# Kernel optimization log

Measured on AMD Instinct MI355X. Metric: run time of the kernel, lower is better.

The kernel has to match this reference:

```python
import jax, jax.numpy as jnp
import numpy as np

B, T, D, H = 4, 2048, 1024, 16
DK = DV = 64
R = 64
KS = 4
EPS = 1e-6


def setup_inputs() -> dict:
    key = jax.random.key(0)
    ks = jax.random.split(key, 16)
    def w(k, shape, s=0.02):
        return jax.random.normal(k, shape, jnp.float32) * s
    return {
        "x": jax.random.normal(ks[0], (B, T, D), jnp.float32),
        "conv_q_w": w(ks[1], (D, 1, KS), 0.3), "conv_q_b": jnp.zeros((D,), jnp.float32),
        "conv_k_w": w(ks[2], (D, 1, KS), 0.3), "conv_k_b": jnp.zeros((D,), jnp.float32),
        "conv_v_w": w(ks[3], (D, 1, KS), 0.3), "conv_v_b": jnp.zeros((D,), jnp.float32),
        "Wq": w(ks[4], (D, H * DK)), "bq": jnp.zeros((H * DK,), jnp.float32),
        "Wk": w(ks[5], (D, H * DK)), "bk": jnp.zeros((H * DK,), jnp.float32),
        "Wv": w(ks[6], (D, H * DV)), "bv": jnp.zeros((H * DV,), jnp.float32),
        "W_ad": w(ks[7], (D, R)), "b_ad": jnp.zeros((R,), jnp.float32),
        "W_au": w(ks[8], (R, H * DK)), "b_au": jnp.zeros((H * DK,), jnp.float32),
        "W_beta": w(ks[9], (D, H)), "b_beta": jnp.zeros((H,), jnp.float32),
        "rms_w": jnp.ones((H, DV), jnp.float32),
        "W_gd": w(ks[10], (D, R)), "b_gd": jnp.zeros((R,), jnp.float32),
        "W_gu": w(ks[11], (R, H)), "b_gu": jnp.zeros((H,), jnp.float32),
        "Wo": w(ks[12], (H * DV, D)), "bo": jnp.zeros((D,), jnp.float32),
    }


def _shortconv(x, w, b):
    # causal depthwise conv1d: torch pads (KS-1) both sides then slices [:T] == left-pad KS-1
    xc = jnp.transpose(x, (0, 2, 1))  # [B, D, T]
    y = jax.lax.conv_general_dilated(
        xc, w, (1,), [(KS - 1, 0)],
        dimension_numbers=("NCH", "OIH", "NCH"), feature_group_count=D)
    y = y + b[None, :, None]
    return jax.nn.silu(jnp.transpose(y, (0, 2, 1)))  # [B, T, D]


def _l2(x):
    # x / sqrt(clamp(sum(x^2), eps))  (matches torch clamp_min then sqrt)
    return x / jnp.sqrt(jnp.maximum(jnp.sum(x * x, -1, keepdims=True), EPS))


def _heads(z, dh):
    # [B,T,H*dh] -> [B*H,T,dh]
    return jnp.transpose(z.reshape(B, T, H, dh), (0, 2, 1, 3)).reshape(B * H, T, dh)


def reference(x, conv_q_w, conv_q_b, conv_k_w, conv_k_b, conv_v_w, conv_v_b,
              Wq, bq, Wk, bk, Wv, bv, W_ad, b_ad, W_au, b_au, W_beta, b_beta,
              rms_w, W_gd, b_gd, W_gu, b_gu, Wo, bo):
    qx = _shortconv(x, conv_q_w, conv_q_b)
    kx = _shortconv(x, conv_k_w, conv_k_b)
    vx = _shortconv(x, conv_v_w, conv_v_b)
    Q = _l2(_heads(qx @ Wq + bq, DK))            # [BH,T,DK]
    K = _l2(_heads(kx @ Wk + bk, DK))            # [BH,T,DK]
    V = _heads(vx @ Wv + bv, DV)                 # [BH,T,DV]
    alpha = jax.nn.sigmoid(jax.nn.silu(x @ W_ad + b_ad) @ W_au + b_au)  # [B,T,H*DK]
    A = _heads(alpha, DK)                        # [BH,T,DK]
    beta = jax.nn.sigmoid(x @ W_beta + b_beta)   # [B,T,H]
    Bta = jnp.transpose(beta, (0, 2, 1)).reshape(B * H, T, 1)

    S0 = jnp.zeros((B * H, DK, DV), jnp.float32)

    def step(S, inp):
        q, k, v, a, b = inp                      # [BH,DK],[BH,DK],[BH,DV],[BH,DK],[BH,1]
        S = S * a[:, :, None]                    # gated decay (row scale)
        kTS = jnp.einsum("bi,bij->bj", k, S)    # k^T S : [BH,DV]
        S = S + (b * k)[:, :, None] * (v - kTS)[:, None, :]  # rank-1 delta update
        o = jnp.einsum("bij,bi->bj", S, q)      # S^T q : [BH,DV]
        return S, o

    tm = lambda z: jnp.transpose(z, (1, 0, 2))   # time-major for scan
    S_final, out_t = jax.lax.scan(step, S0, (tm(Q), tm(K), tm(V), tm(A), tm(Bta)))
    O = jnp.transpose(out_t, (1, 0, 2)).reshape(B, H, T, DV)

    # headwise RMSNorm then sigmoid output gate
    var = jnp.mean(O * O, -1, keepdims=True)
    O = O * jax.lax.rsqrt(var + EPS) * rms_w[None, :, None, :]
    gate = jax.nn.sigmoid(jax.nn.silu(x @ W_gd + b_gd) @ W_gu + b_gu)  # [B,T,H]
    O = O * jnp.transpose(gate, (0, 2, 1))[:, :, :, None]

    y = jnp.transpose(O, (0, 2, 1, 3)).reshape(B, T, H * DV) @ Wo + bo
    return y, S_final.reshape(B, H, DK, DV)
```

## Files before the change

kernel.cpp:

```cpp
#include <hip/hip_runtime.h>
#include <hip/hip_bf16.h>
#include <cstdint>

#define BB 4
#define TT 2048
#define DD 1024
#define HH 16
#define NR (BB*TT)
#define CC 16
#define NCH (TT/CC)

typedef __attribute__((ext_vector_type(8))) short bf16x8;
typedef __attribute__((ext_vector_type(4))) float f32x4;
typedef __attribute__((ext_vector_type(2))) float f32x2;
typedef __attribute__((ext_vector_type(4))) unsigned int u32x4;
typedef __attribute__((ext_vector_type(2))) unsigned int u32x2;

#define GLL(g, l, SZ) __builtin_amdgcn_global_load_lds( \
    (const __attribute__((address_space(1))) void*)(uintptr_t)(const void*)(g), \
    (__attribute__((address_space(3))) void*)(uintptr_t)(void*)(l), SZ, 0, 0)

__device__ __forceinline__ unsigned short f2bf(float f) {
  unsigned u = __builtin_bit_cast(unsigned, f);
  unsigned r = 0x7FFFu + ((u >> 16) & 1u);
  return (unsigned short)((u + r) >> 16);
}
__device__ __forceinline__ unsigned pk2(float a, float b) {
  return (unsigned)f2bf(a) | ((unsigned)f2bf(b) << 16);
}
__device__ __forceinline__ float siluf(float v) { return v / (1.f + __expf(-v)); }
__device__ __forceinline__ float sigmf(float v) { return 1.f / (1.f + __expf(-v)); }

__global__ __launch_bounds__(256) void prep_weights(
    const float* __restrict__ Wq, const float* __restrict__ Wk,
    const float* __restrict__ Wv, const float* __restrict__ Wo,
    unsigned short* __restrict__ WqT, unsigned short* __restrict__ WkT,
    unsigned short* __restrict__ WvT, unsigned short* __restrict__ WoT,
    const float* __restrict__ Wau, unsigned short* __restrict__ WauT,
    const float* __restrict__ Wad, const float* __restrict__ Wgd,
    const float* __restrict__ Wbeta, unsigned short* __restrict__ Wst1T,
    const float* __restrict__ Wgu, unsigned short* __restrict__ WguT,
    const float* __restrict__ bad, const float* __restrict__ bgd,
    const float* __restrict__ bbeta, const float* __restrict__ bgu,
    float* __restrict__ bst1, float* __restrict__ bgup) {
  const int blk = (int)blockIdx.x;
  const int tid = threadIdx.x;
  if (blk < 1024) {
    __shared__ float tile[64][65];
    const int which = blk >> 8, sub = blk & 255;
    const float* W = (which == 0) ? Wq : (which == 1) ? Wk : (which == 2) ? Wv : Wo;
    unsigned short* Wt = (which == 0) ? WqT : (which == 1) ? WkT : (which == 2) ? WvT : WoT;
    const int bk = (sub & 15) * 64, bn = (sub >> 4) * 64;
    const int r = tid >> 2, c4 = (tid & 3) * 16;
#pragma unroll 4
    for (int e = 0; e < 16; ++e)
      tile[r][c4 + e] = W[(size_t)(bk + r) * 1024 + bn + c4 + e];
    __syncthreads();
#pragma unroll 4
    for (int e = 0; e < 16; ++e)
      Wt[(size_t)(bn + r) * 1024 + bk + c4 + e] = f2bf(tile[c4 + e][r]);
  } else if (blk < 1280) {
    int idx = (blk - 1024) * 256 + tid;
    int n = idx >> 6, k = idx & 63;
    WauT[idx] = f2bf(Wau[(size_t)k * 1024 + n]);
  } else if (blk < 2304) {
    int idx = (blk - 1280) * 256 + tid;
    int n = idx >> 10, k = idx & 1023;
    float v = 0.f;
    if (n < 64) v = Wad[(size_t)k * 64 + n];
    else if (n < 128) v = Wgd[(size_t)k * 64 + (n - 64)];
    else if (n < 144) v = Wbeta[(size_t)k * 16 + (n - 128)];
    Wst1T[idx] = f2bf(v);
  } else if (blk < 2336) {
    int idx = (blk - 2304) * 256 + tid;
    int n = idx >> 6, k = idx & 63;
    float v = (n < 16) ? Wgu[(size_t)k * 16 + n] : 0.f;
    WguT[idx] = f2bf(v);
  } else {
    float v = 0.f;
    if (tid < 64) v = bad[tid];
    else if (tid < 128) v = bgd[tid - 64];
    else if (tid < 144) v = bbeta[tid - 128];
    bst1[tid] = v;
    if (tid < 128) bgup[tid] = (tid < 16) ? bgu[tid] : 0.f;
  }
}

__global__ __launch_bounds__(256) void conv_silu(
    const float* __restrict__ x,
    const float* __restrict__ qw, const float* __restrict__ qb,
    const float* __restrict__ kw, const float* __restrict__ kb,
    const float* __restrict__ vw, const float* __restrict__ vb,
    unsigned short* __restrict__ qx, unsigned short* __restrict__ kx,
    unsigned short* __restrict__ vx, unsigned short* __restrict__ xb) {
  const int n = blockIdx.x;
  const int t = n & (TT - 1);
  const int d0 = threadIdx.x * 4;
  const size_t base = (size_t)n * DD + d0;
  f32x4 zero = {0.f, 0.f, 0.f, 0.f};
  f32x4 x0 = *(const f32x4*)(x + base);
  f32x4 xm1 = (t >= 1) ? *(const f32x4*)(x + base - DD) : zero;
  f32x4 xm2 = (t >= 2) ? *(const f32x4*)(x + base - 2 * DD) : zero;
  f32x4 xm3 = (t >= 3) ? *(const f32x4*)(x + base - 3 * DD) : zero;
  float sq[4], sk[4], sv[4];
#pragma unroll
  for (int e = 0; e < 4; ++e) {
    const int d = d0 + e;
    const f32x4 wq = *(const f32x4*)(qw + (size_t)d * 4);
    const f32x4 wk = *(const f32x4*)(kw + (size_t)d * 4);
    const f32x4 wv = *(const f32x4*)(vw + (size_t)d * 4);
    float aq = wq[0] * xm3[e] + wq[1] * xm2[e] + wq[2] * xm1[e] + wq[3] * x0[e] + qb[d];
    float ak = wk[0] * xm3[e] + wk[1] * xm2[e] + wk[2] * xm1[e] + wk[3] * x0[e] + kb[d];
    float av = wv[0] * xm3[e] + wv[1] * xm2[e] + wv[2] * xm1[e] + wv[3] * x0[e] + vb[d];
    sq[e] = siluf(aq); sk[e] = siluf(ak); sv[e] = siluf(av);
  }
  u32x2 o;
  o[0] = pk2(sq[0], sq[1]); o[1] = pk2(sq[2], sq[3]); *(u32x2*)(qx + base) = o;
  o[0] = pk2(sk[0], sk[1]); o[1] = pk2(sk[2], sk[3]); *(u32x2*)(kx + base) = o;
  o[0] = pk2(sv[0], sv[1]); o[1] = pk2(sv[2], sv[3]); *(u32x2*)(vx + base) = o;
  o[0] = pk2(x0[0], x0[1]); o[1] = pk2(x0[2], x0[3]); *(u32x2*)(xb + base) = o;
}

template <int ACT>
__global__ __launch_bounds__(256) void gemm_bt(
    const unsigned short* __restrict__ A, const unsigned short* __restrict__ Bt,
    const float* __restrict__ bias, float* __restrict__ C,
    int M, int N, int K, int ldc, int nstore) {
  __shared__ unsigned short lsA[128 * 32];
  __shared__ unsigned short lsB[128 * 32];
  const int tid = threadIdx.x;
  const int wid = tid >> 6, lane = tid & 63;
  const int wr = wid >> 1, wc = wid & 1;
  int bx = blockIdx.x, by = blockIdx.y;
  {
    const int nwg = gridDim.x * gridDim.y;
    if ((nwg & 7) == 0) {
      const int flat = by * gridDim.x + bx;
      const int cpx = nwg >> 3;
      const int nf = (flat & 7) * cpx + (flat >> 3);
      bx = nf % gridDim.x;
      by = nf / gridDim.x;
    }
  }
  const int m0 = bx * 128, n0 = by * 128;
  f32x4 acc[4][4] = {};
  const int nk = K >> 5;
  const int r0 = wid * 32 + (lane >> 2);
  const int cb = (lane & 3) * 16;
  char* lA = (char*)lsA;
  char* lB = (char*)lsB;
  const size_t rowb = (size_t)K * 2;

  for (int kt = 0; kt < nk; ++kt) {
    const char* gA = (const char*)(A + (size_t)(m0 + r0) * K) + kt * 64 + cb;
    const char* gB = (const char*)(Bt + (size_t)(n0 + r0) * K) + kt * 64 + cb;
    GLL(gA, lA + (wid * 32) * 64, 16);
    GLL(gA + 16 * rowb, lA + (wid * 32 + 16) * 64, 16);
    GLL(gB, lB + (wid * 32) * 64, 16);
    GLL(gB + 16 * rowb, lB + (wid * 32 + 16) * 64, 16);
    __syncthreads();
    bf16x8 af[4], bfr[4];
#pragma unroll
    for (int f = 0; f < 4; ++f)
      af[f] = *(const bf16x8*)(lA + (wr * 64 + f * 16 + (lane & 15)) * 64 + (lane >> 4) * 16);
#pragma unroll
    for (int f = 0; f < 4; ++f)
      bfr[f] = *(const bf16x8*)(lB + (wc * 64 + f * 16 + (lane & 15)) * 64 + (lane >> 4) * 16);
#pragma unroll
    for (int i = 0; i < 4; ++i)
#pragma unroll
      for (int j = 0; j < 4; ++j)
        acc[i][j] = __builtin_amdgcn_mfma_f32_16x16x32_bf16(af[i], bfr[j], acc[i][j], 0, 0, 0);
    __syncthreads();
  }

  if (ACT == 2) {
#pragma unroll
    for (int i = 0; i < 4; ++i) {
      float ss[4] = {0.f, 0.f, 0.f, 0.f};
#pragma unroll
      for (int j = 0; j < 4; ++j) {
        const int gc = n0 + wc * 64 + j * 16 + (lane & 15);
        const float bv = bias[gc];
#pragma unroll
        for (int r = 0; r < 4; ++r) {
          float v = acc[i][j][r] + bv;
          acc[i][j][r] = v;
          ss[r] = fmaf(v, v, ss[r]);
        }
      }
#pragma unroll
      for (int r = 0; r < 4; ++r) {
        float s = ss[r];
        s += __shfl_xor(s, 1);
        s += __shfl_xor(s, 2);
        s += __shfl_xor(s, 4);
        s += __shfl_xor(s, 8);
        ss[r] = 1.f / sqrtf(fmaxf(s, 1e-6f));
      }
      const int gr0 = m0 + wr * 64 + i * 16 + (lane >> 4) * 4;
#pragma unroll
      for (int j = 0; j < 4; ++j) {
        const int gc = n0 + wc * 64 + j * 16 + (lane & 15);
#pragma unroll
        for (int r = 0; r < 4; ++r)
          C[(size_t)(gr0 + r) * ldc + gc] = acc[i][j][r] * ss[r];
      }
    }
    return;
  }

#pragma unroll
  for (int i = 0; i < 4; ++i) {
    const int gr0 = m0 + wr * 64 + i * 16 + (lane >> 4) * 4;
#pragma unroll
    for (int j = 0; j < 4; ++j) {
      const int gc = n0 + wc * 64 + j * 16 + (lane & 15);
      if (gc < nstore) {
        const float bv = bias[gc];
#pragma unroll
        for (int r = 0; r < 4; ++r) {
          float v = acc[i][j][r] + bv;
          if (ACT == 1) v = sigmf(v);
          C[(size_t)(gr0 + r) * ldc + gc] = v;
        }
      }
    }
  }
}

__global__ __launch_bounds__(256) void gemm_stage1(
    const unsigned short* __restrict__ A, const unsigned short* __restrict__ Bt,
    const float* __restrict__ bias,
    unsigned short* __restrict__ adb, unsigned short* __restrict__ gdb,
    float* __restrict__ betaT) {
  __shared__ unsigned short lsA[128 * 32];
  __shared__ unsigned short lsB[128 * 32];
  const int tid = threadIdx.x;
  const int wid = tid >> 6, lane = tid & 63;
  const int wr = wid >> 1, wc = wid & 1;
  int bx = blockIdx.x, by = blockIdx.y;
  {
    const int nwg = gridDim.x * gridDim.y;
    const int flat = by * gridDim.x + bx;
    const int cpx = nwg >> 3;
    const int nf = (flat & 7) * cpx + (flat >> 3);
    bx = nf % gridDim.x;
    by = nf / gridDim.x;
  }
  const int m0 = bx * 128, n0 = by * 128;
  const int K = 1024;
  f32x4 acc[4][4] = {};
  const int r0 = wid * 32 + (lane >> 2);
  const int cb = (lane & 3) * 16;
  char* lA = (char*)lsA;
  char* lB = (char*)lsB;
  const size_t rowb = (size_t)K * 2;

  for (int kt = 0; kt < 32; ++kt) {
    const char* gA = (const char*)(A + (size_t)(m0 + r0) * K) + kt * 64 + cb;
    const char* gB = (const char*)(Bt + (size_t)(n0 + r0) * K) + kt * 64 + cb;
    GLL(gA, lA + (wid * 32) * 64, 16);
    GLL(gA + 16 * rowb, lA + (wid * 32 + 16) * 64, 16);
    GLL(gB, lB + (wid * 32) * 64, 16);
    GLL(gB + 16 * rowb, lB + (wid * 32 + 16) * 64, 16);
    __syncthreads();
    bf16x8 af[4], bfr[4];
#pragma unroll
    for (int f = 0; f < 4; ++f)
      af[f] = *(const bf16x8*)(lA + (wr * 64 + f * 16 + (lane & 15)) * 64 + (lane >> 4) * 16);
#pragma unroll
    for (int f = 0; f < 4; ++f)
      bfr[f] = *(const bf16x8*)(lB + (wc * 64 + f * 16 + (lane & 15)) * 64 + (lane >> 4) * 16);
#pragma unroll
    for (int i = 0; i < 4; ++i)
#pragma unroll
      for (int j = 0; j < 4; ++j)
        acc[i][j] = __builtin_amdgcn_mfma_f32_16x16x32_bf16(af[i], bfr[j], acc[i][j], 0, 0, 0);
    __syncthreads();
  }

#pragma unroll
  for (int i = 0; i < 4; ++i) {
    const int gr0 = m0 + wr * 64 + i * 16 + (lane >> 4) * 4;
#pragma unroll
    for (int j = 0; j < 4; ++j) {
      const int gc = n0 + wc * 64 + j * 16 + (lane & 15);
      if (gc >= 144) continue;
      const float bv = bias[gc];
#pragma unroll
      for (int r = 0; r < 4; ++r) {
        const int row = gr0 + r;
        float v = acc[i][j][r] + bv;
        if (gc < 64) {
          adb[(size_t)row * 64 + gc] = f2bf(siluf(v));
        } else if (gc < 128) {
          gdb[(size_t)row * 64 + (gc - 64)] = f2bf(siluf(v));
        } else {
          int bb = row >> 11, tt = row & (TT - 1);
          betaT[((size_t)(bb * HH + (gc - 128))) * TT + tt] = sigmf(v);
        }
      }
    }
  }
}

__global__ __launch_bounds__(256) void scan_phaseA(
    float* __restrict__ Qn, float* __restrict__ Kn, float* __restrict__ Vv,
    float* __restrict__ Alp, const float* __restrict__ betaT,
    float* __restrict__ Pbuf, float* __restrict__ bCbuf) {
  __shared__ float bA[CC][68], bKt[CC][68], bKp[CC][68], bQ[CC][68];
  __shared__ float bW1[CC][68], bW2[CC][68], bU1[CC][68], bU2[CC][68];
  __shared__ float Nm[CC][20], Nt[CC][20];
  __shared__ float bet[CC];
  const int bid = (int)blockIdx.x;
  const int bh = bid >> 7, c = bid & 127;
  const int b = bh >> 4, h = bh & 15;
  const int tid = threadIdx.x;
  const int tG = tid >> 4, sA = tid & 15, dG = sA * 4;
  const size_t seg = ((size_t)b * TT) * DD + h * 64;
  const size_t off = seg + (size_t)(c * CC + tG) * DD + dG;

  *(f32x4*)&bA [tG][dG] = *(const f32x4*)(Alp + off);
  *(f32x4*)&bKt[tG][dG] = *(const f32x4*)(Kn  + off);
  *(f32x4*)&bW1[tG][dG] = *(const f32x4*)(Vv  + off);
  *(f32x4*)&bQ [tG][dG] = *(const f32x4*)(Qn  + off);
  if (tid < CC) bet[tid] = betaT[(size_t)bh * TT + c * CC + tid];
  __syncthreads();

  if (tid < 64) {
    float p = bA[0][tid];
#pragma unroll
    for (int t = 1; t < CC; ++t) { p *= bA[t][tid]; bA[t][tid] = p; }
  }
  __syncthreads();

  {
    f32x4 bb = *(f32x4*)&bA[tG][dG];
    f32x4 kk = *(f32x4*)&bKt[tG][dG];
    f32x4 qq = *(f32x4*)&bQ[tG][dG];
    f32x4 vv = *(f32x4*)&bW1[tG][dG];
    f32x4 bC = *(f32x4*)&bA[CC - 1][dG];
    const float bt = bet[tG];
    f32x4 kt, kp, qt, w1, w2, kb;
#pragma unroll
    for (int e = 0; e < 4; ++e) {
      float inv = 1.0f / bb[e];
      kt[e] = kk[e] * bb[e];
      kp[e] = kk[e] * inv;
      qt[e] = qq[e] * bb[e];
      w1[e] = bt * vv[e];
      w2[e] = bt * kt[e];
      kb[e] = kp[e] * bC[e];
    }
    *(f32x4*)&bKt[tG][dG] = kt;
    *(f32x4*)&bKp[tG][dG] = kp;
    *(f32x4*)&bQ [tG][dG] = qt;
    *(f32x4*)&bW1[tG][dG] = w1;
    *(f32x4*)&bW2[tG][dG] = w2;
    *(f32x4*)(Qn + off) = qt;
    *(f32x4*)(Alp + off) = kb;
    if (tid < 64) bCbuf[((size_t)bh * 128 + c) * 64 + tid] = bA[CC - 1][tid];
  }
  __syncthreads();

  {
    f32x4 da = {0.f, 0.f, 0.f, 0.f}, dp = {0.f, 0.f, 0.f, 0.f};
#pragma unroll
    for (int ii = 0; ii < 16; ++ii) {
      f32x4 y = *(f32x4*)&bKp[sA][ii * 4];
      da += (*(f32x4*)&bKt[tG][ii * 4]) * y;
      dp += (*(f32x4*)&bQ [tG][ii * 4]) * y;
    }
    float dotA = (da[0] + da[1]) + (da[2] + da[3]);
    float dotP = (dp[0] + dp[1]) + (dp[2] + dp[3]);
    Nm[tG][sA] = (sA < tG) ? (-bet[tG] * dotA) : 0.f;
    Pbuf[((size_t)bh * 128 + c) * 256 + tG * 16 + sA] = (sA <= tG) ? dotP : 0.f;
  }
  __syncthreads();

#define NEUM2(Pw, I1, I2, O1, O2)                                        \
    {                                                                    \
      f32x4 a1 = *(f32x4*)&I1[tG][dG];                                   \
      f32x4 a2 = *(f32x4*)&I2[tG][dG];                                   \
      for (int s4 = 0; s4 < 4; ++s4) {                                   \
        f32x4 pv = *(f32x4*)&Pw[tG][s4 * 4];                             \
        _Pragma("unroll")                                                \
        for (int e = 0; e < 4; ++e) {                                    \
          a1 += pv[e] * (*(f32x4*)&I1[s4 * 4 + e][dG]);                  \
          a2 += pv[e] * (*(f32x4*)&I2[s4 * 4 + e][dG]);                  \
        }                                                                \
      }                                                                  \
      *(f32x4*)&O1[tG][dG] = a1;                                         \
      *(f32x4*)&O2[tG][dG] = a2;                                         \
    }
#define SQMAT(Pw, Pout)                                                  \
    {                                                                    \
      float acc = 0.f;                                                   \
      _Pragma("unroll")                                                  \
      for (int s = 0; s < 16; ++s) acc = fmaf(Pw[tG][s], Pw[s][sA], acc);\
      Pout[tG][sA] = acc;                                                \
    }

  NEUM2(Nm, bW1, bW2, bU1, bU2)
  SQMAT(Nm, Nt)
  __syncthreads();
  NEUM2(Nt, bU1, bU2, bW1, bW2)
  SQMAT(Nt, Nm)
  __syncthreads();
  NEUM2(Nm, bW1, bW2, bU1, bU2)
  SQMAT(Nm, Nt)
  __syncthreads();
  {
    f32x4 a1 = *(f32x4*)&bU1[tG][dG];
    f32x4 a2 = *(f32x4*)&bU2[tG][dG];
    for (int s4 = 0; s4 < 4; ++s4) {
      f32x4 pv = *(f32x4*)&Nt[tG][s4 * 4];
#pragma unroll
      for (int e = 0; e < 4; ++e) {
        a1 += pv[e] * (*(f32x4*)&bU1[s4 * 4 + e][dG]);
        a2 += pv[e] * (*(f32x4*)&bU2[s4 * 4 + e][dG]);
      }
    }
    *(f32x4*)(Vv + off) = a1;
    *(f32x4*)(Kn + off) = a2;
  }
#undef NEUM2
#undef SQMAT
}

__global__ __launch_bounds__(512, 2) void scan_phaseB(
    const float* __restrict__ W1g, const float* __restrict__ W2g,
    const float* __restrict__ Qt, const float* __restrict__ Kb,
    const float* __restrict__ Pbuf, const float* __restrict__ bCbuf,
    float* __restrict__ O, float* __restrict__ Sout) {
  __shared__ float S0T[16][68];
  __shared__ float pU [16][17][2];
  __shared__ float pOq[16][17][2];
  __shared__ float pw2[2][16][68];
  __shared__ float pqt[2][16][68];
  __shared__ float pkb[2][16][68];
  __shared__ float pP [2][16][20];
  __shared__ float pbC[2][64];
  const int blk = (int)blockIdx.x;
  const int bh = blk & 63, cg = blk >> 6;
  const int b = bh >> 4, hh = bh & 15;
  const int tid = threadIdx.x;
  const int h = tid >> 8;
  const int t8 = tid & 255;
  const int T = t8 >> 4, j = t8 & 15;
  const int jg = cg * 16 + j;
  const size_t seg = ((size_t)b * TT) * DD + hh * 64;

  const int qr = t8 >> 4, qc = t8 & 15;

#define PLOAD(c, W2R, QTR, KBR, PR, BCR, W1R)                               \
  {                                                                         \
    const size_t rb = seg + (size_t)((c) * CC + qr) * DD + qc * 4;          \
    if (h == 0) {                                                           \
      W2R = *(const f32x4*)(W2g + rb);                                      \
      QTR = *(const f32x4*)(Qt + rb);                                       \
      W1R = W1g[seg + (size_t)((c) * CC + T) * DD + jg];                    \
    } else {                                                                \
      KBR = *(const f32x4*)(Kb + rb);                                       \
      PR  = Pbuf[((size_t)bh * 128 + (c)) * 256 + t8];                      \
      BCR = (t8 < 64) ? bCbuf[((size_t)bh * 128 + (c)) * 64 + t8] : 0.f;    \
    }                                                                       \
  }
#define PSTORE(bufI, W2R, QTR, KBR, PR, BCR)                                \
  {                                                                         \
    if (h == 0) {                                                           \
      *(f32x4*)&pw2[bufI][qr][qc * 4] = W2R;                                \
      *(f32x4*)&pqt[bufI][qr][qc * 4] = QTR;                                \
    } else {                                                                \
      *(f32x4*)&pkb[bufI][qr][qc * 4] = KBR;                                \
      pP[bufI][qr][qc] = PR;                                                \
      if (t8 < 64) pbC[bufI][t8] = BCR;                                     \
    }                                                                       \
  }

  f32x4 w2r = {}, qtr = {}, kbr = {};
  float pr = 0.f, bcr = 0.f, w1l = 0.f;
  PLOAD(0, w2r, qtr, kbr, pr, bcr, w1l)
  PSTORE(0, w2r, qtr, kbr, pr, bcr)
  {
    int e0 = tid, e1 = tid + 512;
    S0T[e0 >> 6][e0 & 63] = 0.f;
    S0T[e1 >> 6][e1 & 63] = 0.f;
  }
  __syncthreads();

  for (int c = 0; c < NCH; ++c) {
    const int buf = c & 1;
    f32x4 w2n = {}, qtn = {}, kbn = {};
    float pn = 0.f, bcn = 0.f, w1n = 0.f;
    const bool more = (c + 1 < NCH);
    if (more) PLOAD(c + 1, w2n, qtn, kbn, pn, bcn, w1n)

    float u0 = (h == 0) ? w1l : 0.f, u1 = 0.f, q0 = 0.f, q1 = 0.f;
#pragma unroll
    for (int k4 = 0; k4 < 8; ++k4) {
      const int kk = h * 32 + k4 * 4;
      f32x4 wv = *(const f32x4*)&pw2[buf][T][kk];
      f32x4 qv = *(const f32x4*)&pqt[buf][T][kk];
      f32x4 sv = *(const f32x4*)&S0T[j][kk];
      u0 = fmaf(-wv[0], sv[0], u0); q0 = fmaf(qv[0], sv[0], q0);
      u1 = fmaf(-wv[1], sv[1], u1); q1 = fmaf(qv[1], sv[1], q1);
      u0 = fmaf(-wv[2], sv[2], u0); q0 = fmaf(qv[2], sv[2], q0);
      u1 = fmaf(-wv[3], sv[3], u1); q1 = fmaf(qv[3], sv[3], q1);
    }
    pU[T][j][h] = u0 + u1;
    pOq[T][j][h] = q0 + q1;
    __syncthreads();

    float um[CC];
#pragma unroll
    for (int s = 0; s < CC; ++s) {
      f32x2 t2 = *(const f32x2*)&pU[s][j][0];
      um[s] = t2[0] + t2[1];
    }

    if (h == 0) {
      f32x2 oq2 = *(const f32x2*)&pOq[T][j][0];
      float o = oq2[0] + oq2[1];
#pragma unroll
      for (int s4 = 0; s4 < 4; ++s4) {
        f32x4 pv = *(const f32x4*)&pP[buf][T][s4 * 4];
        o = fmaf(pv[0], um[s4 * 4 + 0], o);
        o = fmaf(pv[1], um[s4 * 4 + 1], o);
        o = fmaf(pv[2], um[s4 * 4 + 2], o);
        o = fmaf(pv[3], um[s4 * 4 + 3], o);
      }
      O[seg + (size_t)(c * CC + T) * DD + jg] = o;
    }

    {
      const int r0 = 4 * T + 2 * h;
      f32x2 bcv = *(const f32x2*)&pbC[buf][r0];
      f32x2 s2 = *(const f32x2*)&S0T[j][r0];
      float sp0 = bcv[0] * s2[0];
      float sp1 = bcv[1] * s2[1];
#pragma unroll
      for (int s = 0; s < CC; ++s) {
        f32x2 kv = *(const f32x2*)&pkb[buf][s][r0];
        sp0 = fmaf(kv[0], um[s], sp0);
        sp1 = fmaf(kv[1], um[s], sp1);
      }
      f32x2 so = {sp0, sp1};
      *(f32x2*)&S0T[j][r0] = so;
    }

    if (more) PSTORE(buf ^ 1, w2n, qtn, kbn, pn, bcn)
    __syncthreads();
    w1l = w1n;
  }
#undef PLOAD
#undef PSTORE

  {
    const int r0 = 4 * T + 2 * h;
    f32x2 s2 = *(const f32x2*)&S0T[j][r0];
    Sout[(size_t)bh * 4096 + (size_t)(r0 + 0) * 64 + jg] = s2[0];
    Sout[(size_t)bh * 4096 + (size_t)(r0 + 1) * 64 + jg] = s2[1];
  }
}

__global__ __launch_bounds__(256) void rms_gate(
    const float* __restrict__ O, const float* __restrict__ rmsw,
    const float* __restrict__ gate, unsigned short* __restrict__ Og) {
  const int tid = threadIdx.x;
  const int row = blockIdx.x * 4 + (tid >> 6);
  const int lane = tid & 63;
  const int h = lane >> 2;
  const float* p = O + (size_t)row * DD + lane * 16;
  f32x4 v[4];
  float ss = 0.f;
#pragma unroll
  for (int u = 0; u < 4; ++u) {
    v[u] = *(const f32x4*)(p + u * 4);
#pragma unroll
    for (int e = 0; e < 4; ++e) ss = fmaf(v[u][e], v[u][e], ss);
  }
  ss += __shfl_xor(ss, 1);
  ss += __shfl_xor(ss, 2);
  const float rs = rsqrtf(ss * (1.f / 64.f) + 1e-6f);
  const float g = gate[row * 16 + h];
  const float* wp = rmsw + h * 64 + (lane & 3) * 16;
  unsigned ow[8];
#pragma unroll
  for (int u = 0; u < 4; ++u) {
    f32x4 wv = *(const f32x4*)(wp + u * 4);
    float a0 = v[u][0] * rs * wv[0] * g, a1 = v[u][1] * rs * wv[1] * g;
    float a2 = v[u][2] * rs * wv[2] * g, a3 = v[u][3] * rs * wv[3] * g;
    ow[u * 2] = pk2(a0, a1);
    ow[u * 2 + 1] = pk2(a2, a3);
  }
  u32x4* dst = (u32x4*)(Og + (size_t)row * DD + lane * 16);
  u32x4 o1, o2;
  o1[0] = ow[0]; o1[1] = ow[1]; o1[2] = ow[2]; o1[3] = ow[3];
  o2[0] = ow[4]; o2[1] = ow[5]; o2[2] = ow[6]; o2[3] = ow[7];
  dst[0] = o1; dst[1] = o2;
}

extern "C" void kernel_launch(void* const* d_in, const int* in_sizes, int n_in,
                              void* d_out, int out_size, void* d_ws, size_t ws_size,
                              hipStream_t stream) {
  const float* x    = (const float*)d_in[0];
  const float* qw   = (const float*)d_in[1];
  const float* qb   = (const float*)d_in[2];
  const float* kw   = (const float*)d_in[3];
  const float* kb   = (const float*)d_in[4];
  const float* vw   = (const float*)d_in[5];
  const float* vb   = (const float*)d_in[6];
  const float* Wq   = (const float*)d_in[7];
  const float* bq   = (const float*)d_in[8];
  const float* Wk   = (const float*)d_in[9];
  const float* bk   = (const float*)d_in[10];
  const float* Wv   = (const float*)d_in[11];
  const float* bv   = (const float*)d_in[12];
  const float* Wad  = (const float*)d_in[13];
  const float* bad  = (const float*)d_in[14];
  const float* Wau  = (const float*)d_in[15];
  const float* bau  = (const float*)d_in[16];
  const float* Wbeta= (const float*)d_in[17];
  const float* bbeta= (const float*)d_in[18];
  const float* rmsw = (const float*)d_in[19];
  const float* Wgd  = (const float*)d_in[20];
  const float* bgd  = (const float*)d_in[21];
  const float* Wgu  = (const float*)d_in[22];
  const float* bgu  = (const float*)d_in[23];
  const float* Wo   = (const float*)d_in[24];
  const float* bo   = (const float*)d_in[25];

  char* ws = (char*)d_ws;
  const size_t MB = 1ull << 20;
  unsigned short* WqT   = (unsigned short*)(ws + 0 * MB);
  unsigned short* WkT   = (unsigned short*)(ws + 2 * MB);
  unsigned short* WvT   = (unsigned short*)(ws + 4 * MB);
  unsigned short* WoT   = (unsigned short*)(ws + 6 * MB);
  unsigned short* WauT  = (unsigned short*)(ws + 8 * MB);
  unsigned short* Wst1T = (unsigned short*)(ws + 8 * MB + 256 * 1024);
  unsigned short* WguT  = (unsigned short*)(ws + 8 * MB + 768 * 1024);
  float* bst1 = (float*)(ws + 8 * MB + 800 * 1024);
  float* bgup = (float*)(ws + 8 * MB + 804 * 1024);
  unsigned short* x_bf = (unsigned short*)(ws + 9 * MB);
  unsigned short* qx   = (unsigned short*)(ws + 25 * MB);
  unsigned short* kx   = (unsigned short*)(ws + 41 * MB);
  unsigned short* vx   = (unsigned short*)(ws + 57 * MB);
  float* Qn    = (float*)(ws + 73 * MB);
  float* Kn    = (float*)(ws + 105 * MB);
  float* Vv    = (float*)(ws + 137 * MB);
  float* stage1= (float*)(ws + 169 * MB);
  unsigned short* adb = (unsigned short*)(ws + 177 * MB);
  unsigned short* gdb = (unsigned short*)(ws + 178 * MB);
  float* betaT = (float*)(ws + 179 * MB);
  float* gate  = (float*)(ws + 179 * MB + 512 * 1024);
  float* bCbuf = (float*)(ws + 180 * MB);
  float* alpha = (float*)(ws + 9 * MB);
  float* Obuf  = (float*)(ws + 41 * MB);
  unsigned short* Og = (unsigned short*)(ws + 137 * MB);
  float* Pbuf  = stage1;
  float* y = (float*)d_out;
  float* Sout = y + (size_t)NR * DD;

  dim3 blk(256);
  prep_weights<<<dim3(2337), blk, 0, stream>>>(
      Wq, Wk, Wv, Wo, WqT, WkT, WvT, WoT,
      Wau, WauT, Wad, Wgd, Wbeta, Wst1T, Wgu, WguT,
      bad, bgd, bbeta, bgu, bst1, bgup);

  conv_silu<<<dim3(NR), blk, 0, stream>>>(x, qw, qb, kw, kb, vw, vb, qx, kx, vx, x_bf);

  gemm_stage1<<<dim3(64, 2), blk, 0, stream>>>(x_bf, Wst1T, bst1, adb, gdb, betaT);
  gemm_bt<2><<<dim3(64, 8), blk, 0, stream>>>(qx, WqT, bq, Qn, NR, 1024, 1024, 1024, 1024);
  gemm_bt<2><<<dim3(64, 8), blk, 0, stream>>>(kx, WkT, bk, Kn, NR, 1024, 1024, 1024, 1024);
  gemm_bt<0><<<dim3(64, 8), blk, 0, stream>>>(vx, WvT, bv, Vv, NR, 1024, 1024, 1024, 1024);
  gemm_bt<1><<<dim3(64, 8), blk, 0, stream>>>(adb, WauT, bau, alpha, NR, 1024, 64, 1024, 1024);
  gemm_bt<1><<<dim3(64, 1), blk, 0, stream>>>(gdb, WguT, bgup, gate, NR, 128, 64, 16, 16);

  scan_phaseA<<<dim3(8192), blk, 0, stream>>>(Qn, Kn, Vv, alpha, betaT, Pbuf, bCbuf);
  scan_phaseB<<<dim3(256), dim3(512), 0, stream>>>(Vv, Kn, Qn, alpha, Pbuf, bCbuf, Obuf, Sout);

  rms_gate<<<dim3(2048), blk, 0, stream>>>(Obuf, rmsw, gate, Og);
  gemm_bt<0><<<dim3(64, 8), blk, 0, stream>>>(Og, WoT, bo, y, NR, 1024, 1024, 1024, 1024);
}
```

Before: 492.3 us.

## Fuse conv into weight prep kernel and form chunk inverse before applying

Merges the depthwise conv/SiLU kernel into the weight-prep kernel as one launch, which saves a kernel launch and its tail. In phase A, the Neumann-series inverse (I+N)^-1 is now built as a 16x16 matrix by repeated squaring. It is then applied once to W1/W2, instead of multiplying the 16x64 operands at every step. This cuts LDS traffic and FLOPs in the triangular solve and frees two shared buffers, with a small change in floating-point summation order.

```diff
diff --git a/kernel.cpp b/kernel.cpp
--- a/kernel.cpp
+++ b/kernel.cpp
@@ -31,7 +31,13 @@
 __device__ __forceinline__ float siluf(float v) { return v / (1.f + __expf(-v)); }
 __device__ __forceinline__ float sigmf(float v) { return 1.f / (1.f + __expf(-v)); }
 
-__global__ __launch_bounds__(256) void prep_weights(
+__global__ __launch_bounds__(256) void prologue(
+    const float* __restrict__ x,
+    const float* __restrict__ qw, const float* __restrict__ qb,
+    const float* __restrict__ kw, const float* __restrict__ kb,
+    const float* __restrict__ vw, const float* __restrict__ vb,
+    unsigned short* __restrict__ qx, unsigned short* __restrict__ kx,
+    unsigned short* __restrict__ vx, unsigned short* __restrict__ xb,
     const float* __restrict__ Wq, const float* __restrict__ Wk,
     const float* __restrict__ Wv, const float* __restrict__ Wo,
     unsigned short* __restrict__ WqT, unsigned short* __restrict__ WkT,
@@ -43,8 +49,38 @@
     const float* __restrict__ bad, const float* __restrict__ bgd,
     const float* __restrict__ bbeta, const float* __restrict__ bgu,
     float* __restrict__ bst1, float* __restrict__ bgup) {
-  const int blk = (int)blockIdx.x;
+  const int blk0 = (int)blockIdx.x;
   const int tid = threadIdx.x;
+  if (blk0 < NR) {
+    const int n = blk0;
+    const int t = n & (TT - 1);
+    const int d0 = tid * 4;
+    const size_t base = (size_t)n * DD + d0;
+    f32x4 zero = {0.f, 0.f, 0.f, 0.f};
+    f32x4 x0 = *(const f32x4*)(x + base);
+    f32x4 xm1 = (t >= 1) ? *(const f32x4*)(x + base - DD) : zero;
+    f32x4 xm2 = (t >= 2) ? *(const f32x4*)(x + base - 2 * DD) : zero;
+    f32x4 xm3 = (t >= 3) ? *(const f32x4*)(x + base - 3 * DD) : zero;
+    float sq[4], sk[4], sv[4];
+#pragma unroll
+    for (int e = 0; e < 4; ++e) {
+      const int d = d0 + e;
+      const f32x4 wq = *(const f32x4*)(qw + (size_t)d * 4);
+      const f32x4 wk = *(const f32x4*)(kw + (size_t)d * 4);
+      const f32x4 wv = *(const f32x4*)(vw + (size_t)d * 4);
+      float aq = wq[0] * xm3[e] + wq[1] * xm2[e] + wq[2] * xm1[e] + wq[3] * x0[e] + qb[d];
+      float ak = wk[0] * xm3[e] + wk[1] * xm2[e] + wk[2] * xm1[e] + wk[3] * x0[e] + kb[d];
+      float av = wv[0] * xm3[e] + wv[1] * xm2[e] + wv[2] * xm1[e] + wv[3] * x0[e] + vb[d];
+      sq[e] = siluf(aq); sk[e] = siluf(ak); sv[e] = siluf(av);
+    }
+    u32x2 o;
+    o[0] = pk2(sq[0], sq[1]); o[1] = pk2(sq[2], sq[3]); *(u32x2*)(qx + base) = o;
+    o[0] = pk2(sk[0], sk[1]); o[1] = pk2(sk[2], sk[3]); *(u32x2*)(kx + base) = o;
+    o[0] = pk2(sv[0], sv[1]); o[1] = pk2(sv[2], sv[3]); *(u32x2*)(vx + base) = o;
+    o[0] = pk2(x0[0], x0[1]); o[1] = pk2(x0[2], x0[3]); *(u32x2*)(xb + base) = o;
+    return;
+  }
+  const int blk = blk0 - NR;
   if (blk < 1024) {
     __shared__ float tile[64][65];
     const int which = blk >> 8, sub = blk & 255;
@@ -86,41 +122,6 @@
   }
 }
 
-__global__ __launch_bounds__(256) void conv_silu(
-    const float* __restrict__ x,
-    const float* __restrict__ qw, const float* __restrict__ qb,
-    const float* __restrict__ kw, const float* __restrict__ kb,
-    const float* __restrict__ vw, const float* __restrict__ vb,
-    unsigned short* __restrict__ qx, unsigned short* __restrict__ kx,
-    unsigned short* __restrict__ vx, unsigned short* __restrict__ xb) {
-  const int n = blockIdx.x;
-  const int t = n & (TT - 1);
-  const int d0 = threadIdx.x * 4;
-  const size_t base = (size_t)n * DD + d0;
-  f32x4 zero = {0.f, 0.f, 0.f, 0.f};
-  f32x4 x0 = *(const f32x4*)(x + base);
-  f32x4 xm1 = (t >= 1) ? *(const f32x4*)(x + base - DD) : zero;
-  f32x4 xm2 = (t >= 2) ? *(const f32x4*)(x + base - 2 * DD) : zero;
-  f32x4 xm3 = (t >= 3) ? *(const f32x4*)(x + base - 3 * DD) : zero;
-  float sq[4], sk[4], sv[4];
-#pragma unroll
-  for (int e = 0; e < 4; ++e) {
-    const int d = d0 + e;
-    const f32x4 wq = *(const f32x4*)(qw + (size_t)d * 4);
-    const f32x4 wk = *(const f32x4*)(kw + (size_t)d * 4);
-    const f32x4 wv = *(const f32x4*)(vw + (size_t)d * 4);
-    float aq = wq[0] * xm3[e] + wq[1] * xm2[e] + wq[2] * xm1[e] + wq[3] * x0[e] + qb[d];
-    float ak = wk[0] * xm3[e] + wk[1] * xm2[e] + wk[2] * xm1[e] + wk[3] * x0[e] + kb[d];
-    float av = wv[0] * xm3[e] + wv[1] * xm2[e] + wv[2] * xm1[e] + wv[3] * x0[e] + vb[d];
-    sq[e] = siluf(aq); sk[e] = siluf(ak); sv[e] = siluf(av);
-  }
-  u32x2 o;
-  o[0] = pk2(sq[0], sq[1]); o[1] = pk2(sq[2], sq[3]); *(u32x2*)(qx + base) = o;
-  o[0] = pk2(sk[0], sk[1]); o[1] = pk2(sk[2], sk[3]); *(u32x2*)(kx + base) = o;
-  o[0] = pk2(sv[0], sv[1]); o[1] = pk2(sv[2], sv[3]); *(u32x2*)(vx + base) = o;
-  o[0] = pk2(x0[0], x0[1]); o[1] = pk2(x0[2], x0[3]); *(u32x2*)(xb + base) = o;
-}
-
 template <int ACT>
 __global__ __launch_bounds__(256) void gemm_bt(
     const unsigned short* __restrict__ A, const unsigned short* __restrict__ Bt,
@@ -310,8 +311,9 @@
     float* __restrict__ Alp, const float* __restrict__ betaT,
     float* __restrict__ Pbuf, float* __restrict__ bCbuf) {
   __shared__ float bA[CC][68], bKt[CC][68], bKp[CC][68], bQ[CC][68];
-  __shared__ float bW1[CC][68], bW2[CC][68], bU1[CC][68], bU2[CC][68];
+  __shared__ float bW1[CC][68], bW2[CC][68];
   __shared__ float Nm[CC][20], Nt[CC][20];
+  __shared__ float Ta[CC][20], Tb[CC][20];
   __shared__ float bet[CC];
   const int bid = (int)blockIdx.x;
   const int bh = bid >> 7, c = bid & 127;
@@ -374,59 +376,62 @@
     }
     float dotA = (da[0] + da[1]) + (da[2] + da[3]);
     float dotP = (dp[0] + dp[1]) + (dp[2] + dp[3]);
-    Nm[tG][sA] = (sA < tG) ? (-bet[tG] * dotA) : 0.f;
+    const float nval = (sA < tG) ? (-bet[tG] * dotA) : 0.f;
+    Nm[tG][sA] = nval;
+    Ta[tG][sA] = nval + ((sA == tG) ? 1.f : 0.f);
     Pbuf[((size_t)bh * 128 + c) * 256 + tG * 16 + sA] = (sA <= tG) ? dotP : 0.f;
   }
   __syncthreads();
 
-#define NEUM2(Pw, I1, I2, O1, O2)                                        \
-    {                                                                    \
-      f32x4 a1 = *(f32x4*)&I1[tG][dG];                                   \
-      f32x4 a2 = *(f32x4*)&I2[tG][dG];                                   \
-      for (int s4 = 0; s4 < 4; ++s4) {                                   \
-        f32x4 pv = *(f32x4*)&Pw[tG][s4 * 4];                             \
-        _Pragma("unroll")                                                \
-        for (int e = 0; e < 4; ++e) {                                    \
-          a1 += pv[e] * (*(f32x4*)&I1[s4 * 4 + e][dG]);                  \
-          a2 += pv[e] * (*(f32x4*)&I2[s4 * 4 + e][dG]);                  \
-        }                                                                \
-      }                                                                  \
-      *(f32x4*)&O1[tG][dG] = a1;                                         \
-      *(f32x4*)&O2[tG][dG] = a2;                                         \
-    }
-#define SQMAT(Pw, Pout)                                                  \
-    {                                                                    \
-      float acc = 0.f;                                                   \
-      _Pragma("unroll")                                                  \
-      for (int s = 0; s < 16; ++s) acc = fmaf(Pw[tG][s], Pw[s][sA], acc);\
-      Pout[tG][sA] = acc;                                                \
-    }
-
-  NEUM2(Nm, bW1, bW2, bU1, bU2)
-  SQMAT(Nm, Nt)
-  __syncthreads();
-  NEUM2(Nt, bU1, bU2, bW1, bW2)
-  SQMAT(Nt, Nm)
-  __syncthreads();
-  NEUM2(Nm, bW1, bW2, bU1, bU2)
-  SQMAT(Nm, Nt)
-  __syncthreads();
-  {
-    f32x4 a1 = *(f32x4*)&bU1[tG][dG];
-    f32x4 a2 = *(f32x4*)&bU2[tG][dG];
+  {
+    float sq = 0.f;
+#pragma unroll
+    for (int s = 0; s < 16; ++s) sq = fmaf(Nm[tG][s], Nm[s][sA], sq);
+    Nt[tG][sA] = sq;
+  }
+  __syncthreads();
+  {
+    float acc = Ta[tG][sA], sq = 0.f;
+#pragma unroll
+    for (int s = 0; s < 16; ++s) {
+      acc = fmaf(Nt[tG][s], Ta[s][sA], acc);
+      sq = fmaf(Nt[tG][s], Nt[s][sA], sq);
+    }
+    Tb[tG][sA] = acc;
+    Nm[tG][sA] = sq;
+  }
+  __syncthreads();
+  {
+    float acc = Tb[tG][sA], sq = 0.f;
+#pragma unroll
+    for (int s = 0; s < 16; ++s) {
+      acc = fmaf(Nm[tG][s], Tb[s][sA], acc);
+      sq = fmaf(Nm[tG][s], Nm[s][sA], sq);
+    }
+    Ta[tG][sA] = acc;
+    Nt[tG][sA] = sq;
+  }
+  __syncthreads();
+  {
+    float acc = Ta[tG][sA];
+#pragma unroll
+    for (int s = 0; s < 16; ++s) acc = fmaf(Nt[tG][s], Ta[s][sA], acc);
+    Tb[tG][sA] = acc;
+  }
+  __syncthreads();
+  {
+    f32x4 a1 = {0.f, 0.f, 0.f, 0.f}, a2 = {0.f, 0.f, 0.f, 0.f};
     for (int s4 = 0; s4 < 4; ++s4) {
-      f32x4 pv = *(f32x4*)&Nt[tG][s4 * 4];
+      f32x4 tv = *(f32x4*)&Tb[tG][s4 * 4];
 #pragma unroll
       for (int e = 0; e < 4; ++e) {
-        a1 += pv[e] * (*(f32x4*)&bU1[s4 * 4 + e][dG]);
-        a2 += pv[e] * (*(f32x4*)&bU2[s4 * 4 + e][dG]);
+        a1 += tv[e] * (*(f32x4*)&bW1[s4 * 4 + e][dG]);
+        a2 += tv[e] * (*(f32x4*)&bW2[s4 * 4 + e][dG]);
       }
     }
     *(f32x4*)(Vv + off) = a1;
     *(f32x4*)(Kn + off) = a2;
   }
-#undef NEUM2
-#undef SQMAT
 }
 
 __global__ __launch_bounds__(512, 2) void scan_phaseB(
@@ -664,12 +669,11 @@
   float* Sout = y + (size_t)NR * DD;
 
   dim3 blk(256);
-  prep_weights<<<dim3(2337), blk, 0, stream>>>(
+  prologue<<<dim3(NR + 2337), blk, 0, stream>>>(
+      x, qw, qb, kw, kb, vw, vb, qx, kx, vx, x_bf,
       Wq, Wk, Wv, Wo, WqT, WkT, WvT, WoT,
       Wau, WauT, Wad, Wgd, Wbeta, Wst1T, Wgu, WguT,
       bad, bgd, bbeta, bgu, bst1, bgup);
-
-  conv_silu<<<dim3(NR), blk, 0, stream>>>(x, qw, qb, kw, kb, vw, vb, qx, kx, vx, x_bf);
 
   gemm_stage1<<<dim3(64, 2), blk, 0, stream>>>(x_bf, Wst1T, bst1, adb, gdb, betaT);
   gemm_bt<2><<<dim3(64, 8), blk, 0, stream>>>(qx, WqT, bq, Qn, NR, 1024, 1024, 1024, 1024);
```

After: 465.4 us. -5.5%, faster.
